# Optimization experiments

Hardware: AMD Instinct MI355X
Metric: run time of the kernel (lower is better)

## Reference

```python
import jax, jax.numpy as jnp
import numpy as np

# ---- module config (matches __init__ defaults) ----
NUM_EL_FULL = 128
LV_START, LV_END = 31, 95
NUM_S = LV_END - LV_START            # 64 sensors
NX = NY = 408
ROI = 128
DX = DY = 0.0002
C0 = 1500.0
FS = 40.0e6
DT = 1.0 / FS
R_IN = 0.0406
ARC_ANGLE = 270.0
ARC_START = 135.0
T_SAMPLES = 2030
BATCH = 64


def _geometry():
    """Reproduce _precompute_geometry + _precompute_time_indices_and_weights in numpy."""
    spacing = ARC_ANGLE / (NUM_EL_FULL - 1)
    all_ang = ARC_START + np.arange(NUM_EL_FULL) * spacing
    ang = all_ang[LV_START:LV_END]
    ang_rad = ang * np.pi / 180.0
    cx = (NX / 2 - 0.5) * DX
    cy = (NY / 2 - 0.5) * DY
    sx = cx + R_IN * np.cos(ang_rad)
    sy = cy + R_IN * np.sin(ang_rad)

    rsx = round((NX - ROI) / 2)
    rsy = round((NY - ROI) / 2)
    x_pos = (np.arange(rsx, rsx + ROI, dtype=np.float32) * DX)
    y_pos = (np.arange(rsy, rsy + ROI, dtype=np.float32) * DY)
    yg, xg = np.meshgrid(y_pos, x_pos, indexing='ij')  # [ROI, ROI]

    x_diff = xg[..., None] - sx[None, None, :]          # [ROI, ROI, S]
    y_diff = yg[..., None] - sy[None, None, :]
    dist = np.sqrt(x_diff ** 2 + y_diff ** 2)
    t_idx = np.round(dist / C0 / DT).astype(np.int32)

    normal = ang_rad + np.pi
    a2p = np.arctan2(y_diff, x_diff)
    adiff = a2p - normal[None, None, :]
    adiff = np.arctan2(np.sin(adiff), np.cos(adiff))
    weights = np.clip(np.cos(adiff), 0.0, None).astype(np.float32)
    valid = (t_idx >= 0) & (t_idx < T_SAMPLES)
    return t_idx, weights, valid


def setup_inputs() -> dict:
    key = jax.random.key(0)
    t_idx, weights, valid = _geometry()
    sinogram = jax.random.normal(key, (BATCH, 1, NUM_S, T_SAMPLES), dtype=jnp.float32)
    return {
        "sinogram": sinogram,
        "weights": jnp.asarray(weights),
        "time_indices": jnp.asarray(t_idx),
        "valid_mask": jnp.asarray(valid),
    }


def reference(sinogram, weights, time_indices, valid_mask):
    """DAS beamforming, output_type='both', norm_type='clamp'."""
    B = sinogram.shape[0]
    T = sinogram.shape[-1]
    sino = sinogram[:, 0]                                   # [B, S, T]
    S = sino.shape[1]
    t = jnp.clip(time_indices, 0, T - 1)                    # [H, W, S]
    sensor_idx = jnp.arange(S)[None, None, :]               # [1, 1, S]
    # gather: per-pixel, per-sensor time sample -> [B, H, W, S]
    sampled = sino[:, sensor_idx, t]
    w = jnp.where(valid_mask, weights, 0.0)                 # mask * weight fused
    weighted = sampled * w[None]                            # [B, H, W, S]

    das = weighted.sum(axis=3)[:, None]                     # [B, 1, H, W]
    # normalize: clamp to >=0, per-batch max
    das = jnp.maximum(das, 0.0)
    m = das.reshape(B, -1).max(axis=1)
    m = jnp.where(m > 1e-8, m, 1.0)
    das = das / m[:, None, None, None]

    pixel_interp = jnp.transpose(weighted, (0, 3, 1, 2))    # [B, S, H, W]
    return das, pixel_interp
```

## Files before the change

kernel.cpp:

```cpp
#include <hip/hip_runtime.h>
#include <stdint.h>

#define NB   64
#define NS   64
#define NT   2030
#define NP   16384
#define DAS_ELEMS (NB * NP)

typedef float v4f __attribute__((ext_vector_type(4)));

__global__ __launch_bounds__(256) void prep_kernel(
    const int* __restrict__ t_idx, const float* __restrict__ w,
    unsigned short* __restrict__ tc, float* __restrict__ wv)
{
    __shared__ int   ti[64][65];
    __shared__ float wf[64][65];
    const int pbase = blockIdx.x * 64;

    #pragma unroll
    for (int k = 0; k < 16; ++k) {
        int o = k * 256 + threadIdx.x;
        int r = o >> 6, s = o & 63;
        ti[r][s] = t_idx[pbase * 64 + o];
        wf[r][s] = w[pbase * 64 + o];
    }
    __syncthreads();

    #pragma unroll
    for (int k = 0; k < 16; ++k) {
        int o = k * 256 + threadIdx.x;
        int s = o >> 6, r = o & 63;
        int t = ti[r][s];
        bool valid = (t >= 0) & (t < NT);
        int tcl = min(max(t, 0), NT - 1);
        tc[s * NP + pbase + r] = (unsigned short)tcl;
        wv[s * NP + pbase + r] = valid ? wf[r][s] : 0.0f;
    }
}

__global__ __launch_bounds__(256) void main_strided_kernel(
    const float* __restrict__ sino,
    const unsigned short* __restrict__ tptr,
    const float* __restrict__ wptr,
    float*       __restrict__ das,
    float*       __restrict__ pix,
    unsigned*    __restrict__ bmax)
{
    const int tid = threadIdx.x;
    const int p   = blockIdx.x * 512 + tid;
    const int b0  = blockIdx.y * 2, b1 = b0 + 1;
    const float* __restrict__ sr0 = sino + (size_t)b0 * (NS * NT);
    const float* __restrict__ sr1 = sino + (size_t)b1 * (NS * NT);
    float* __restrict__ pix0 = pix + ((size_t)b0 * NS) * NP + p;
    float* __restrict__ pix1 = pix + ((size_t)b1 * NS) * NP + p;

    float a00 = 0.f, a01 = 0.f, a10 = 0.f, a11 = 0.f;

    int t0, t1; float w0, w1;
    {
        const unsigned short* tp = tptr + p;
        const float*          wp = wptr + p;
        t0 = tp[0]; t1 = tp[256];
        w0 = wp[0]; w1 = wp[256];
    }

    for (int s = 0; s < NS; ++s) {
        int nt0 = 0, nt1 = 0; float nw0 = 0.f, nw1 = 0.f;
        if (s + 1 < NS) {
            const unsigned short* tp = tptr + (s + 1) * NP + p;
            const float*          wp = wptr + (s + 1) * NP + p;
            nt0 = tp[0]; nt1 = tp[256];
            nw0 = wp[0]; nw1 = wp[256];
        }

        const float* __restrict__ r0 = sr0 + s * NT;
        const float* __restrict__ r1 = sr1 + s * NT;
        float v00 = r0[t0] * w0;
        float v01 = r0[t1] * w1;
        float v10 = r1[t0] * w0;
        float v11 = r1[t1] * w1;

        float* q0 = pix0 + (size_t)s * NP;
        float* q1 = pix1 + (size_t)s * NP;
        __builtin_nontemporal_store(v00, q0);
        __builtin_nontemporal_store(v01, q0 + 256);
        __builtin_nontemporal_store(v10, q1);
        __builtin_nontemporal_store(v11, q1 + 256);

        a00 += v00; a01 += v01; a10 += v10; a11 += v11;

        t0 = nt0; t1 = nt1; w0 = nw0; w1 = nw1;
    }

    a00 = fmaxf(a00, 0.f); a01 = fmaxf(a01, 0.f);
    a10 = fmaxf(a10, 0.f); a11 = fmaxf(a11, 0.f);
    das[(size_t)b0 * NP + p]       = a00;
    das[(size_t)b0 * NP + p + 256] = a01;
    das[(size_t)b1 * NP + p]       = a10;
    das[(size_t)b1 * NP + p + 256] = a11;

    float m0 = fmaxf(a00, a01);
    float m1 = fmaxf(a10, a11);
    #pragma unroll
    for (int off = 32; off > 0; off >>= 1) {
        m0 = fmaxf(m0, __shfl_down(m0, off, 64));
        m1 = fmaxf(m1, __shfl_down(m1, off, 64));
    }
    __shared__ float wm0[4], wm1[4];
    const int wid = tid >> 6, lane = tid & 63;
    if (lane == 0) { wm0[wid] = m0; wm1[wid] = m1; }
    __syncthreads();
    if (tid == 0) {
        m0 = fmaxf(fmaxf(wm0[0], wm0[1]), fmaxf(wm0[2], wm0[3]));
        m1 = fmaxf(fmaxf(wm1[0], wm1[1]), fmaxf(wm1[2], wm1[3]));
        atomicMax(&bmax[b0], __float_as_uint(m0));
        atomicMax(&bmax[b1], __float_as_uint(m1));
    }
}

__global__ __launch_bounds__(256) void main_fallback_kernel(
    const float* __restrict__ sino,
    const int*   __restrict__ tptr,
    const float* __restrict__ wptr,
    float*       __restrict__ das,
    float*       __restrict__ pix,
    unsigned*    __restrict__ bmax)
{
    const int b = blockIdx.y;
    const int p = blockIdx.x * 1024 + threadIdx.x * 4;
    const float* __restrict__ srow = sino + (size_t)b * (NS * NT);
    float* __restrict__ pixb = pix + (size_t)b * ((size_t)NS * NP) + p;

    v4f acc = (v4f)(0.0f);

    for (int s = 0; s < NS; ++s) {
        int t0 = tptr[(p + 0) * NS + s];
        int t1 = tptr[(p + 1) * NS + s];
        int t2 = tptr[(p + 2) * NS + s];
        int t3 = tptr[(p + 3) * NS + s];
        float wx = ((t0 >= 0) & (t0 < NT)) ? wptr[(p + 0) * NS + s] : 0.f;
        float wy = ((t1 >= 0) & (t1 < NT)) ? wptr[(p + 1) * NS + s] : 0.f;
        float wz = ((t2 >= 0) & (t2 < NT)) ? wptr[(p + 2) * NS + s] : 0.f;
        float ww = ((t3 >= 0) & (t3 < NT)) ? wptr[(p + 3) * NS + s] : 0.f;
        int4 t;
        t.x = min(max(t0, 0), NT - 1);
        t.y = min(max(t1, 0), NT - 1);
        t.z = min(max(t2, 0), NT - 1);
        t.w = min(max(t3, 0), NT - 1);
        const float* __restrict__ sr = srow + s * NT;
        v4f v;
        v.x = sr[t.x] * wx;
        v.y = sr[t.y] * wy;
        v.z = sr[t.z] * wz;
        v.w = sr[t.w] * ww;
        __builtin_nontemporal_store(v, (v4f*)(pixb + (size_t)s * NP));
        acc += v;
    }

    acc.x = fmaxf(acc.x, 0.f); acc.y = fmaxf(acc.y, 0.f);
    acc.z = fmaxf(acc.z, 0.f); acc.w = fmaxf(acc.w, 0.f);
    *(v4f*)(das + (size_t)b * NP + p) = acc;

    float m = fmaxf(fmaxf(acc.x, acc.y), fmaxf(acc.z, acc.w));
    #pragma unroll
    for (int off = 32; off > 0; off >>= 1)
        m = fmaxf(m, __shfl_down(m, off, 64));
    __shared__ float wm[4];
    if ((threadIdx.x & 63) == 0) wm[threadIdx.x >> 6] = m;
    __syncthreads();
    if (threadIdx.x == 0) {
        m = fmaxf(fmaxf(wm[0], wm[1]), fmaxf(wm[2], wm[3]));
        atomicMax(&bmax[b], __float_as_uint(m));
    }
}

__global__ __launch_bounds__(256) void norm_kernel(
    float* __restrict__ das, const unsigned* __restrict__ bmax)
{
    int idx = (blockIdx.x * 256 + threadIdx.x) * 4;
    int b = idx >> 14;
    float m = __uint_as_float(bmax[b]);
    m = (m > 1e-8f) ? m : 1.0f;
    v4f v = *(v4f*)(das + idx);
    v.x = v.x / m; v.y = v.y / m; v.z = v.z / m; v.w = v.w / m;
    *(v4f*)(das + idx) = v;
}

extern "C" void kernel_launch(void* const* d_in, const int* in_sizes, int n_in,
                              void* d_out, int out_size, void* d_ws, size_t ws_size,
                              hipStream_t stream)
{
    const float* sino  = (const float*)d_in[0];
    const float* w     = (const float*)d_in[1];
    const int*   t_idx = (const int*)  d_in[2];

    float* das = (float*)d_out;
    float* pix = (float*)d_out + DAS_ELEMS;

    char* ws = (char*)d_ws;
    const size_t need = (size_t)(6u << 20) + 256;
    const bool big = ws_size >= need;

    unsigned* bmax;
    float* wv = nullptr; unsigned short* tc = nullptr;
    if (big) {
        wv   = (float*)ws;
        tc   = (unsigned short*)(ws + (4u << 20));
        bmax = (unsigned*)(ws + (6u << 20));
    } else {
        bmax = (unsigned*)ws;
    }

    (void)hipMemsetAsync(bmax, 0, NB * sizeof(unsigned), stream);

    if (big) {
        prep_kernel<<<256, 256, 0, stream>>>(t_idx, w, tc, wv);
        main_strided_kernel<<<dim3(32, 32), 256, 0, stream>>>(sino, tc, wv, das, pix, bmax);
    } else {
        main_fallback_kernel<<<dim3(16, NB), 256, 0, stream>>>(sino, t_idx, w, das, pix, bmax);
    }
    norm_kernel<<<DAS_ELEMS / 1024, 256, 0, stream>>>(das, bmax);
}
```

Before: 367.2 us.

## Remap blocks so each XCD owns a fixed set of batch pairs for L2 locality

Switches to a 1D grid of 2048 blocks and decodes the block id so that consecutive ids, which the hardware distributes round-robin across the 8 XCDs, land on different XCDs. Each XCD then processes only four batch pairs, so the sinogram rows it gathers from stay in that XCD's private L2. Each thread now handles one pixel instead of two, doubling block count, and the delay/weight tables are read with nontemporal loads. The trade-off is less per-thread work, fewer gathers in flight per thread, and the tables being re-read by every XCD without being kept in cache.

```diff
diff --git a/kernel.cpp b/kernel.cpp
--- a/kernel.cpp
+++ b/kernel.cpp
@@ -38,7 +38,7 @@
     }
 }
 
-__global__ __launch_bounds__(256) void main_strided_kernel(
+__global__ __launch_bounds__(256) void main_l2_kernel(
     const float* __restrict__ sino,
     const unsigned short* __restrict__ tptr,
     const float* __restrict__ wptr,
@@ -46,61 +46,50 @@
     float*       __restrict__ pix,
     unsigned*    __restrict__ bmax)
 {
-    const int tid = threadIdx.x;
-    const int p   = blockIdx.x * 512 + tid;
-    const int b0  = blockIdx.y * 2, b1 = b0 + 1;
+    const int tid  = threadIdx.x;
+    const int bid  = blockIdx.x;
+    const int xcd  = bid & 7;
+    const int j    = bid >> 3;
+    const int tile = j & 63;
+    const int pair = xcd * 4 + (j >> 6);
+    const int b0   = pair * 2, b1 = b0 + 1;
+    const int p    = tile * 256 + tid;
+
     const float* __restrict__ sr0 = sino + (size_t)b0 * (NS * NT);
     const float* __restrict__ sr1 = sino + (size_t)b1 * (NS * NT);
     float* __restrict__ pix0 = pix + ((size_t)b0 * NS) * NP + p;
     float* __restrict__ pix1 = pix + ((size_t)b1 * NS) * NP + p;
 
-    float a00 = 0.f, a01 = 0.f, a10 = 0.f, a11 = 0.f;
-
-    int t0, t1; float w0, w1;
-    {
-        const unsigned short* tp = tptr + p;
-        const float*          wp = wptr + p;
-        t0 = tp[0]; t1 = tp[256];
-        w0 = wp[0]; w1 = wp[256];
-    }
+    float a0 = 0.f, a1 = 0.f;
+
+    int   t = __builtin_nontemporal_load(tptr + p);
+    float w = __builtin_nontemporal_load(wptr + p);
 
     for (int s = 0; s < NS; ++s) {
-        int nt0 = 0, nt1 = 0; float nw0 = 0.f, nw1 = 0.f;
+        int nt = 0; float nw = 0.f;
         if (s + 1 < NS) {
-            const unsigned short* tp = tptr + (s + 1) * NP + p;
-            const float*          wp = wptr + (s + 1) * NP + p;
-            nt0 = tp[0]; nt1 = tp[256];
-            nw0 = wp[0]; nw1 = wp[256];
+            nt = __builtin_nontemporal_load(tptr + (s + 1) * NP + p);
+            nw = __builtin_nontemporal_load(wptr + (s + 1) * NP + p);
         }
 
         const float* __restrict__ r0 = sr0 + s * NT;
         const float* __restrict__ r1 = sr1 + s * NT;
-        float v00 = r0[t0] * w0;
-        float v01 = r0[t1] * w1;
-        float v10 = r1[t0] * w0;
-        float v11 = r1[t1] * w1;
-
-        float* q0 = pix0 + (size_t)s * NP;
-        float* q1 = pix1 + (size_t)s * NP;
-        __builtin_nontemporal_store(v00, q0);
-        __builtin_nontemporal_store(v01, q0 + 256);
-        __builtin_nontemporal_store(v10, q1);
-        __builtin_nontemporal_store(v11, q1 + 256);
-
-        a00 += v00; a01 += v01; a10 += v10; a11 += v11;
-
-        t0 = nt0; t1 = nt1; w0 = nw0; w1 = nw1;
-    }
-
-    a00 = fmaxf(a00, 0.f); a01 = fmaxf(a01, 0.f);
-    a10 = fmaxf(a10, 0.f); a11 = fmaxf(a11, 0.f);
-    das[(size_t)b0 * NP + p]       = a00;
-    das[(size_t)b0 * NP + p + 256] = a01;
-    das[(size_t)b1 * NP + p]       = a10;
-    das[(size_t)b1 * NP + p + 256] = a11;
-
-    float m0 = fmaxf(a00, a01);
-    float m1 = fmaxf(a10, a11);
+        float v0 = r0[t] * w;
+        float v1 = r1[t] * w;
+
+        __builtin_nontemporal_store(v0, pix0 + (size_t)s * NP);
+        __builtin_nontemporal_store(v1, pix1 + (size_t)s * NP);
+
+        a0 += v0; a1 += v1;
+        t = nt; w = nw;
+    }
+
+    a0 = fmaxf(a0, 0.f);
+    a1 = fmaxf(a1, 0.f);
+    das[(size_t)b0 * NP + p] = a0;
+    das[(size_t)b1 * NP + p] = a1;
+
+    float m0 = a0, m1 = a1;
     #pragma unroll
     for (int off = 32; off > 0; off >>= 1) {
         m0 = fmaxf(m0, __shfl_down(m0, off, 64));
@@ -215,7 +204,7 @@
 
     if (big) {
         prep_kernel<<<256, 256, 0, stream>>>(t_idx, w, tc, wv);
-        main_strided_kernel<<<dim3(32, 32), 256, 0, stream>>>(sino, tc, wv, das, pix, bmax);
+        main_l2_kernel<<<2048, 256, 0, stream>>>(sino, tc, wv, das, pix, bmax);
     } else {
         main_fallback_kernel<<<dim3(16, NB), 256, 0, stream>>>(sino, t_idx, w, das, pix, bmax);
     }
```

Measured after the change: 397.1 us. 1.08x slower.
